# Optimization experiments

Measured on AMD Instinct MI355X. Metric: run time of the kernel, lower is better.

The kernel has to match this reference:

```python
import jax, jax.numpy as jnp
import numpy as np

B, S, H, NH = 4, 2048, 1024, 16
HD = H // NH


def setup_inputs() -> dict:
    key = jax.random.key(0)
    ks = jax.random.split(key, 8)
    x = jax.random.normal(ks[0], (B, S, H), dtype=jnp.float32)
    y = jax.random.normal(ks[1], (B, S, H), dtype=jnp.float32)
    mask = jnp.zeros((B, S), dtype=bool)  # key padding mask; True = masked
    s = 0.02
    Wq_w = jax.random.normal(ks[2], (H, H), dtype=jnp.float32) * s
    Wq_b = jnp.zeros((H,), dtype=jnp.float32)
    Wkv_w = jax.random.normal(ks[3], (H, 2 * H), dtype=jnp.float32) * s
    Wkv_b = jnp.zeros((2 * H,), dtype=jnp.float32)
    Wo_w = jax.random.normal(ks[4], (H, H), dtype=jnp.float32) * s
    Wo_b = jnp.zeros((H,), dtype=jnp.float32)
    return {"x": x, "y": y, "mask": mask, "Wq_w": Wq_w, "Wq_b": Wq_b,
            "Wkv_w": Wkv_w, "Wkv_b": Wkv_b, "Wo_w": Wo_w, "Wo_b": Wo_b}


def reference(x, y, mask, Wq_w, Wq_b, Wkv_w, Wkv_b, Wo_w, Wo_b):
    b, s, c = x.shape
    # q: [B, NH, S, HD]
    q = (x @ Wq_w + Wq_b).reshape(b, s, NH, HD).transpose(0, 2, 1, 3)
    # kv: [B, S, 2, NH, HD] -> k, v: [B, NH, S, HD]
    kv = (y @ Wkv_w + Wkv_b).reshape(b, s, 2, NH, HD)
    k = kv[:, :, 0].transpose(0, 2, 1, 3)
    v = kv[:, :, 1].transpose(0, 2, 1, 3)
    attn = jnp.einsum("bhqd,bhkd->bhqk", q, k) / jnp.sqrt(jnp.float32(HD))
    causal = jnp.triu(jnp.ones((s, s), dtype=bool), k=1)  # True above diag = masked
    combined = causal[None, None, :, :] | mask[:, None, None, :]
    attn = jnp.where(combined, -jnp.inf, attn)
    attn = jax.nn.softmax(attn, axis=-1)
    # dropout is identity in eval mode
    out = jnp.einsum("bhqk,bhkd->bhqd", attn, v)
    out = out.transpose(0, 2, 1, 3).reshape(b, s, c)
    return out @ Wo_w + Wo_b
```

## Files before the change

### kernel.cpp

```cpp
#include <hip/hip_runtime.h>


#define Bv   4
#define Sv   2048
#define Hv   1024
#define NHv  16
#define HDv  64

typedef __attribute__((ext_vector_type(8))) short s16x8;
typedef __attribute__((ext_vector_type(4))) short s16x4;
typedef __attribute__((ext_vector_type(4))) float f32x4;

__device__ __forceinline__ short f2bf(float f) {
  unsigned u = __float_as_uint(f);
  unsigned r = (u + 0x7fffu + ((u >> 16) & 1u)) >> 16;
  return (short)r;
}

#if __has_builtin(__builtin_amdgcn_exp2f)
#define EXP2(x) __builtin_amdgcn_exp2f(x)
#else
#define EXP2(x) exp2f(x)
#endif

__device__ __forceinline__ void gl_lds16(const short* g, short* l) {
  __builtin_amdgcn_global_load_lds(
      (const __attribute__((address_space(1))) unsigned int*)g,
      (__attribute__((address_space(3))) unsigned int*)l, 16, 0, 0);
}

__global__ __launch_bounds__(256) void cvt2_bf16(const float* __restrict__ x,
                                                 const float* __restrict__ y,
                                                 short* __restrict__ Xb,
                                                 short* __restrict__ Yb, int nper) {
  int half = gridDim.x >> 1;
  int bid = blockIdx.x;
  const float* in = (bid < half) ? x : y;
  short* out = (bid < half) ? Xb : Yb;
  int lb = (bid < half) ? bid : bid - half;
  int i = (lb * 256 + threadIdx.x) * 4;
  if (i < nper) {
    float4 v = *(const float4*)&in[i];
    short r0 = f2bf(v.x), r1 = f2bf(v.y), r2 = f2bf(v.z), r3 = f2bf(v.w);
    unsigned long long pk = (unsigned long long)(unsigned short)r0
                          | ((unsigned long long)(unsigned short)r1 << 16)
                          | ((unsigned long long)(unsigned short)r2 << 32)
                          | ((unsigned long long)(unsigned short)r3 << 48);
    *(unsigned long long*)&out[i] = pk;
  }
}

__global__ __launch_bounds__(256)
void tcvt3(const float* __restrict__ Wq, const float* __restrict__ Wkv,
           const float* __restrict__ Wo, short* __restrict__ Wt,
           short* __restrict__ Wot) {
  __shared__ float tile[32][33];
  int bx = blockIdx.x;
  const float* in;
  short* out;
  int C, cx;
  if (bx < 32)       { in = Wq;  out = Wt;                          C = 1024; cx = bx; }
  else if (bx < 96)  { in = Wkv; out = Wt + (size_t)Hv * Hv;        C = 2048; cx = bx - 32; }
  else               { in = Wo;  out = Wot;                         C = 1024; cx = bx - 96; }
  const int R = 1024;
  int tx = threadIdx.x & 31, ty = threadIdx.x >> 5;
  int c0 = cx * 32, r0 = blockIdx.y * 32;
#pragma unroll
  for (int i = 0; i < 32; i += 8)
    tile[ty + i][tx] = in[(size_t)(r0 + ty + i) * C + c0 + tx];
  __syncthreads();
#pragma unroll
  for (int i = 0; i < 32; i += 8)
    out[(size_t)(c0 + ty + i) * R + r0 + tx] = f2bf(tile[tx][ty + i]);
}

__global__ __launch_bounds__(256)
void gemm_qkv(const short* __restrict__ Xb, const short* __restrict__ Yb,
              const short* __restrict__ Wt, const float* __restrict__ Wqb,
              const float* __restrict__ Wkvb, short* __restrict__ Qb,
              short* __restrict__ Kb, short* __restrict__ Vt) {
  __shared__ union SMem {
    struct { short A[2][128 * 64]; short B[2][128 * 64]; } g;
    short ep[128 * 136];
  } sm;
  const int tid = threadIdx.x;
  const int w = tid >> 6, l = tid & 63;
  const int wr = w >> 1, wc = w & 1;
  const int m0 = blockIdx.x * 128, n0 = blockIdx.y * 128;
  const short* A = (n0 < 1024) ? Xb : Yb;
  const int sel = n0 >> 10;

  auto STAGE = [&](int k0, int bi) {
#pragma unroll
    for (int i = 0; i < 4; ++i) {
      int c = tid + i * 256;
      int r = c >> 3;
      int u = (c & 7) ^ (r & 7);
      gl_lds16(&A[(size_t)(m0 + r) * Hv + k0 + u * 8], &sm.g.A[bi][c * 8]);
      gl_lds16(&Wt[(size_t)(n0 + r) * Hv + k0 + u * 8], &sm.g.B[bi][c * 8]);
    }
  };

  f32x4 acc[4][4] = {};

  auto KSTEP = [&](int kt) {
    const int buf = kt & 1;
#pragma unroll
    for (int kk = 0; kk < 64; kk += 32) {
      s16x8 af[4], bf[4];
#pragma unroll
      for (int m = 0; m < 4; ++m) {
        int row = wr * 64 + m * 16 + (l & 15);
        int sb = (row * 128 + kk * 2 + ((l >> 4) << 4)) ^ ((row & 7) << 4);
        af[m] = *(s16x8*)((char*)sm.g.A[buf] + sb);
      }
#pragma unroll
      for (int n = 0; n < 4; ++n) {
        int row = wc * 64 + n * 16 + (l & 15);
        int sb = (row * 128 + kk * 2 + ((l >> 4) << 4)) ^ ((row & 7) << 4);
        bf[n] = *(s16x8*)((char*)sm.g.B[buf] + sb);
      }
#pragma unroll
      for (int m = 0; m < 4; ++m)
#pragma unroll
        for (int n = 0; n < 4; ++n)
          acc[m][n] = __builtin_amdgcn_mfma_f32_16x16x32_bf16(af[m], bf[n], acc[m][n], 0, 0, 0);
    }
  };

  STAGE(0, 0);
  STAGE(64, 1);

  for (int kt = 0; kt < 15; ++kt) {
    asm volatile("s_waitcnt vmcnt(8)" ::: "memory");
    __builtin_amdgcn_s_barrier();
    __builtin_amdgcn_sched_barrier(0);
    KSTEP(kt);
    __builtin_amdgcn_s_barrier();
    __builtin_amdgcn_sched_barrier(0);
    if (kt + 2 < 16) STAGE((kt + 2) * 64, kt & 1);
  }
  asm volatile("s_waitcnt vmcnt(0)" ::: "memory");
  __builtin_amdgcn_s_barrier();
  __builtin_amdgcn_sched_barrier(0);
  KSTEP(15);
  __syncthreads();

  const int b = m0 >> 11, s0 = m0 & (Sv - 1);
  if (sel < 2) {
    const float scale = (sel == 0) ? 0.1803368801f : 1.0f;
    const float* bias = (sel == 0) ? Wqb : (Wkvb + (n0 - 1024));
#pragma unroll
    for (int m = 0; m < 4; ++m)
#pragma unroll
      for (int n = 0; n < 4; ++n) {
        int scol = wc * 64 + n * 16 + (l & 15);
#pragma unroll
        for (int e = 0; e < 4; ++e) {
          int srow = wr * 64 + m * 16 + ((l >> 4) << 2) + e;
          float v = (acc[m][n][e] + bias[scol]) * scale;
          sm.ep[srow * 136 + scol] = f2bf(v);
        }
      }
    __syncthreads();
    short* dst = sel ? Kb : Qb;
    const int hbase = (n0 & 1023) >> 6;
#pragma unroll
    for (int p = 0; p < 8; ++p) {
      int u = p * 256 + tid;
      int row = u >> 4, hf = (u >> 3) & 1, sub = u & 7;
      s16x8 vdat = *(s16x8*)&sm.ep[row * 136 + hf * 64 + sub * 8];
      *(s16x8*)&dst[(((size_t)(b * NHv + hbase + hf)) * Sv + s0 + row) * HDv + sub * 8] = vdat;
    }
  } else {
    const float* bias = Wkvb + (n0 - 1024);
#pragma unroll
    for (int m = 0; m < 4; ++m)
#pragma unroll
      for (int n = 0; n < 4; ++n) {
        int scol = wc * 64 + n * 16 + (l & 15);
        int srow0 = wr * 64 + m * 16 + ((l >> 4) << 2);
        s16x4 t;
#pragma unroll
        for (int e = 0; e < 4; ++e) t[e] = f2bf(acc[m][n][e] + bias[scol]);
        *(s16x4*)&sm.ep[scol * 136 + srow0] = t;
      }
    __syncthreads();
    const int hbase = (n0 - 2048) >> 6;
#pragma unroll
    for (int p = 0; p < 8; ++p) {
      int u = p * 256 + tid;
      int col = u >> 4, seg = u & 15;
      s16x8 vdat = *(s16x8*)&sm.ep[col * 136 + seg * 8];
      *(s16x8*)&Vt[(((size_t)(b * NHv + hbase + (col >> 6))) * HDv + (col & 63)) * Sv + s0 + seg * 8] = vdat;
    }
  }
}

__global__ __launch_bounds__(256)
void gemm_out(const short* __restrict__ A, const short* __restrict__ Bt,
              const float* __restrict__ bias, float* __restrict__ outf) {
  __shared__ short Alds[2][128 * 64];
  __shared__ short Blds[2][128 * 64];
  const int tid = threadIdx.x;
  const int w = tid >> 6, l = tid & 63;
  const int wr = w >> 1, wc = w & 1;
  const int m0 = blockIdx.x * 128, n0 = blockIdx.y * 128;

  auto STAGE = [&](int k0, int bi) {
#pragma unroll
    for (int i = 0; i < 4; ++i) {
      int c = tid + i * 256;
      int r = c >> 3;
      int u = (c & 7) ^ (r & 7);
      gl_lds16(&A[(size_t)(m0 + r) * Hv + k0 + u * 8], &Alds[bi][c * 8]);
      gl_lds16(&Bt[(size_t)(n0 + r) * Hv + k0 + u * 8], &Blds[bi][c * 8]);
    }
  };

  f32x4 acc[4][4] = {};

  STAGE(0, 0);
  __syncthreads();
  for (int kt = 0; kt < 16; ++kt) {
    const int buf = kt & 1;
    if (kt < 15) STAGE((kt + 1) * 64, buf ^ 1);
#pragma unroll
    for (int kk = 0; kk < 64; kk += 32) {
      s16x8 af[4], bf[4];
#pragma unroll
      for (int m = 0; m < 4; ++m) {
        int row = wr * 64 + m * 16 + (l & 15);
        int sb = (row * 128 + kk * 2 + ((l >> 4) << 4)) ^ ((row & 7) << 4);
        af[m] = *(s16x8*)((char*)Alds[buf] + sb);
      }
#pragma unroll
      for (int n = 0; n < 4; ++n) {
        int row = wc * 64 + n * 16 + (l & 15);
        int sb = (row * 128 + kk * 2 + ((l >> 4) << 4)) ^ ((row & 7) << 4);
        bf[n] = *(s16x8*)((char*)Blds[buf] + sb);
      }
#pragma unroll
      for (int m = 0; m < 4; ++m)
#pragma unroll
        for (int n = 0; n < 4; ++n)
          acc[m][n] = __builtin_amdgcn_mfma_f32_16x16x32_bf16(af[m], bf[n], acc[m][n], 0, 0, 0);
    }
    __syncthreads();
  }

#pragma unroll
  for (int m = 0; m < 4; ++m)
#pragma unroll
    for (int n = 0; n < 4; ++n)
#pragma unroll
      for (int e = 0; e < 4; ++e) {
        int gr = m0 + wr * 64 + m * 16 + ((l >> 4) << 2) + e;
        int gc = n0 + wc * 64 + n * 16 + (l & 15);
        outf[(size_t)gr * Hv + gc] = acc[m][n][e] + bias[gc];
      }
}

__global__ __launch_bounds__(512)
void attn_mfma(const short* __restrict__ Q, const short* __restrict__ Kb,
               const short* __restrict__ Vt, const unsigned char* __restrict__ msk,
               short* __restrict__ AO) {
  __shared__ short Klds[2][64 * 64];
  __shared__ short Vlds[2][64 * 64];
  __shared__ short Plds[8 * 32 * 64];
  __shared__ unsigned long long mword[2];

  const int tid = threadIdx.x;
  const int w = tid >> 6, l = tid & 63;
  const int il = l & 15, g = l >> 4;
  const int bh = blockIdx.x & 63;
  const int qb = 7 - (blockIdx.x >> 6);
  const int b = bh >> 4, h = bh & 15;
  const int q0 = qb * 256 + w * 32;

  int kvA0[4], pfA0[2];
#pragma unroll
  for (int n = 0; n < 4; ++n) {
    int row = n * 16 + il;
    kvA0[n] = row * 128 + ((g << 4) ^ ((row & 7) << 4));
  }
#pragma unroll
  for (int m = 0; m < 2; ++m) {
    int row = m * 16 + il;
    pfA0[m] = row * 128 + ((g << 4) ^ ((row & 7) << 4));
  }
  const int swzq = (il & 7) << 4;
  const int g8 = g << 3;

  s16x8 qf[2][2];
  const short* qbase = &Q[((size_t)bh * Sv + q0) * HDv];
#pragma unroll
  for (int m = 0; m < 2; ++m)
#pragma unroll
    for (int kk = 0; kk < 2; ++kk)
      qf[m][kk] = *(const s16x8*)&qbase[(m * 16 + il) * 64 + kk * 32 + g8];

  s16x8 onesf;
#pragma unroll
  for (int e2 = 0; e2 < 8; ++e2) onesf[e2] = (short)0x3F80;

  f32x4 oacc[2][4] = {};
  f32x4 lacc[2] = {};
  const f32x4 cinit = {-16.f, -16.f, -16.f, -16.f};

  char* const pbase = (char*)Plds + w * 4096;
  const short* kg0 = &Kb[(size_t)bh * Sv * HDv];
  const short* vg0 = &Vt[(size_t)bh * HDv * Sv];
  const int nkt = qb * 4 + 4;

  auto stageKV = [&](int t, int bufi) {
    const short* kg = kg0 + (size_t)t * 64 * HDv;
    const short* vg = vg0 + t * 64;
    int c = tid;
    int r = c >> 3;
    int u = (c & 7) ^ (r & 7);
    gl_lds16(&kg[(size_t)r * HDv + u * 8], &Klds[bufi][c * 8]);
    gl_lds16(&vg[(size_t)r * Sv + u * 8], &Vlds[bufi][c * 8]);
  };

  stageKV(0, 0);
  if (w == 0) {
    unsigned long long mwb = __ballot(msk[b * Sv + l] != 0);
    if (l == 0) mword[0] = mwb;
  }
  __syncthreads();

  for (int kt = 0; kt < nkt; ++kt) {
    const int k0 = kt * 64;
    const int buf = kt & 1;
    if (kt + 1 < nkt) {
      stageKV(kt + 1, buf ^ 1);
      if (w == 0) {
        unsigned long long mwb = __ballot(msk[b * Sv + (kt + 1) * 64 + l] != 0);
        if (l == 0) mword[buf ^ 1] = mwb;
      }
    }

    if (k0 <= q0 + 31) {
      const unsigned long long mw = mword[buf];
      const char* kldsb = (const char*)Klds[buf];
      const char* vldsb = (const char*)Vlds[buf];
      f32x4 sacc[4][2];
#pragma unroll
      for (int n = 0; n < 4; ++n)
#pragma unroll
        for (int m = 0; m < 2; ++m)
          sacc[n][m] = cinit;
      __builtin_amdgcn_s_setprio(1);
#pragma unroll
      for (int kk = 0; kk < 2; ++kk) {
        s16x8 kf[4];
#pragma unroll
        for (int n = 0; n < 4; ++n)
          kf[n] = *(s16x8*)(kldsb + (kvA0[n] ^ (kk << 6)));
#pragma unroll
        for (int n = 0; n < 4; ++n)
#pragma unroll
          for (int m = 0; m < 2; ++m)
            sacc[n][m] = __builtin_amdgcn_mfma_f32_16x16x32_bf16(kf[n], qf[m][kk], sacc[n][m], 0, 0, 0);
      }
      __builtin_amdgcn_s_setprio(0);

      if ((k0 + 63 > q0) || (mw != 0)) {
#pragma unroll
        for (int n = 0; n < 4; ++n)
#pragma unroll
          for (int m = 0; m < 2; ++m)
#pragma unroll
            for (int e = 0; e < 4; ++e) {
              int klocal = n * 16 + (g << 2) + e;
              int qg = q0 + m * 16 + il;
              bool bad = (k0 + klocal > qg) || ((mw >> klocal) & 1ull);
              if (bad) sacc[n][m][e] = -1e30f;
            }
      }

#pragma unroll
      for (int kk = 0; kk < 2; ++kk) {
#pragma unroll
        for (int m = 0; m < 2; ++m) {
          int pwb = (m * 16 + il) * 128;
#pragma unroll
          for (int n = kk * 2; n < kk * 2 + 2; ++n) {
            s16x4 t;
#pragma unroll
            for (int e = 0; e < 4; ++e) {
              float pv = EXP2(sacc[n][m][e]);
              t[e] = (short)(__float_as_uint(pv) >> 16);
            }
            *(s16x4*)(pbase + pwb + (((n << 5) + g8) ^ swzq)) = t;
          }
        }
        s16x8 pf[2], vf[4];
#pragma unroll
        for (int m = 0; m < 2; ++m)
          pf[m] = *(s16x8*)(pbase + (pfA0[m] ^ (kk << 6)));
#pragma unroll
        for (int n = 0; n < 4; ++n)
          vf[n] = *(s16x8*)(vldsb + (kvA0[n] ^ (kk << 6)));
        __builtin_amdgcn_s_setprio(1);
#pragma unroll
        for (int m = 0; m < 2; ++m) {
#pragma unroll
          for (int n = 0; n < 4; ++n)
            oacc[m][n] = __builtin_amdgcn_mfma_f32_16x16x32_bf16(pf[m], vf[n], oacc[m][n], 0, 0, 0);
          lacc[m] = __builtin_amdgcn_mfma_f32_16x16x32_bf16(pf[m], onesf, lacc[m], 0, 0, 0);
        }
        __builtin_amdgcn_s_setprio(0);
      }
    }
    __syncthreads();
  }

#pragma unroll
  for (int m = 0; m < 2; ++m)
#pragma unroll
    for (int e = 0; e < 4; ++e) {
      float inv = 1.f / lacc[m][e];
#pragma unroll
      for (int n = 0; n < 4; ++n) {
        int qg = q0 + m * 16 + (g << 2) + e;
        int dcol = n * 16 + il;
        AO[((size_t)b * Sv + qg) * Hv + h * HDv + dcol] = f2bf(oacc[m][n][e] * inv);
      }
    }
}

extern "C" void kernel_launch(void* const* d_in, const int* in_sizes, int n_in,
                              void* d_out, int out_size, void* d_ws, size_t ws_size,
                              hipStream_t stream) {
  (void)in_sizes; (void)n_in; (void)out_size; (void)ws_size;
  const float* x    = (const float*)d_in[0];
  const float* y    = (const float*)d_in[1];
  const unsigned char* msk = (const unsigned char*)d_in[2];
  const float* Wq   = (const float*)d_in[3];
  const float* Wqb  = (const float*)d_in[4];
  const float* Wkv  = (const float*)d_in[5];
  const float* Wkvb = (const float*)d_in[6];
  const float* Wo   = (const float*)d_in[7];
  const float* Wob  = (const float*)d_in[8];
  float* out = (float*)d_out;

  char* p = (char*)d_ws;
  auto alloc = [&](size_t bytes) {
    char* r = p;
    p += (bytes + 255) & ~(size_t)255;
    return r;
  };
  const size_t MT = (size_t)Bv * Sv;
  short* Xb   = (short*)alloc(MT * Hv * 2);
  short* Yb   = (short*)alloc(MT * Hv * 2);
  short* Wt   = (short*)alloc((size_t)3 * Hv * Hv * 2);
  short* Wot  = (short*)alloc((size_t)Hv * Hv * 2);
  short* Qb   = (short*)alloc(MT * Hv * 2);
  short* Kb   = (short*)alloc(MT * Hv * 2);
  short* Vb   = (short*)alloc(MT * Hv * 2);
  short* AO   = (short*)alloc(MT * Hv * 2);

  const int n_x = (int)(MT * Hv);
  cvt2_bf16<<<2 * (n_x / 1024), 256, 0, stream>>>(x, y, Xb, Yb, n_x);
  tcvt3<<<dim3(128, 32), 256, 0, stream>>>(Wq, Wkv, Wo, Wt, Wot);

  gemm_qkv<<<dim3(64, 24), 256, 0, stream>>>(Xb, Yb, Wt, Wqb, Wkvb, Qb, Kb, Vb);

  attn_mfma<<<8 * 64, 512, 0, stream>>>(Qb, Kb, Vb, msk, AO);

  gemm_out<<<dim3(64, 8), 256, 0, stream>>>(AO, Wot, Wob, out);
}
```

Before: 158.2 us.

## Deepen GEMM and attention global-to-LDS pipelines with prefetch distance two

Both the projection GEMM and the attention kernel now issue two tiles ahead and wait with partial vmcnt counts plus raw s_barrier, instead of prefetching one tile and using full __syncthreads. The intent is to keep a load in flight across each compute step so global-to-LDS latency is hidden. The attention kernel also drops the shared mask-word LDS staging and has each wave ballot its mask byte directly. The hand-counted vmcnt values must match the number of outstanding loads per thread. The mask load in the compute step adds a global read on the critical path.

```diff
diff --git a/kernel.cpp b/kernel.cpp
--- a/kernel.cpp
+++ b/kernel.cpp
@@ -220,11 +220,8 @@
 
   f32x4 acc[4][4] = {};
 
-  STAGE(0, 0);
-  __syncthreads();
-  for (int kt = 0; kt < 16; ++kt) {
+  auto KSTEP = [&](int kt) {
     const int buf = kt & 1;
-    if (kt < 15) STAGE((kt + 1) * 64, buf ^ 1);
 #pragma unroll
     for (int kk = 0; kk < 64; kk += 32) {
       s16x8 af[4], bf[4];
@@ -246,8 +243,24 @@
         for (int n = 0; n < 4; ++n)
           acc[m][n] = __builtin_amdgcn_mfma_f32_16x16x32_bf16(af[m], bf[n], acc[m][n], 0, 0, 0);
     }
-    __syncthreads();
-  }
+  };
+
+  STAGE(0, 0);
+  STAGE(64, 1);
+
+  for (int kt = 0; kt < 15; ++kt) {
+    asm volatile("s_waitcnt vmcnt(8)" ::: "memory");
+    __builtin_amdgcn_s_barrier();
+    __builtin_amdgcn_sched_barrier(0);
+    KSTEP(kt);
+    __builtin_amdgcn_s_barrier();
+    __builtin_amdgcn_sched_barrier(0);
+    if (kt + 2 < 16) STAGE((kt + 2) * 64, kt & 1);
+  }
+  asm volatile("s_waitcnt vmcnt(0)" ::: "memory");
+  __builtin_amdgcn_s_barrier();
+  __builtin_amdgcn_sched_barrier(0);
+  KSTEP(15);
 
 #pragma unroll
   for (int m = 0; m < 4; ++m)
@@ -268,7 +281,6 @@
   __shared__ short Klds[2][64 * 64];
   __shared__ short Vlds[2][64 * 64];
   __shared__ short Plds[8 * 32 * 64];
-  __shared__ unsigned long long mword[2];
 
   const int tid = threadIdx.x;
   const int w = tid >> 6, l = tid & 63;
@@ -311,6 +323,7 @@
   char* const pbase = (char*)Plds + w * 4096;
   const short* kg0 = &Kb[(size_t)bh * Sv * HDv];
   const short* vg0 = &Vt[(size_t)bh * HDv * Sv];
+  const unsigned char* mrow = &msk[b * Sv + l];
   const int nkt = qb * 4 + 4;
 
   auto stageKV = [&](int t, int bufi) {
@@ -323,99 +336,101 @@
     gl_lds16(&vg[(size_t)r * Sv + u * 8], &Vlds[bufi][c * 8]);
   };
 
-  stageKV(0, 0);
-  if (w == 0) {
-    unsigned long long mwb = __ballot(msk[b * Sv + l] != 0);
-    if (l == 0) mword[0] = mwb;
-  }
-  __syncthreads();
-
-  for (int kt = 0; kt < nkt; ++kt) {
+  auto COMPUTE = [&](int kt) {
     const int k0 = kt * 64;
     const int buf = kt & 1;
-    if (kt + 1 < nkt) {
-      stageKV(kt + 1, buf ^ 1);
-      if (w == 0) {
-        unsigned long long mwb = __ballot(msk[b * Sv + (kt + 1) * 64 + l] != 0);
-        if (l == 0) mword[buf ^ 1] = mwb;
-      }
-    }
-
-    if (k0 <= q0 + 31) {
-      const unsigned long long mw = mword[buf];
-      const char* kldsb = (const char*)Klds[buf];
-      const char* vldsb = (const char*)Vlds[buf];
-      f32x4 sacc[4][2];
+    if (k0 > q0 + 31) return;
+    const unsigned char mb = mrow[k0];
+    const char* kldsb = (const char*)Klds[buf];
+    const char* vldsb = (const char*)Vlds[buf];
+    f32x4 sacc[4][2];
+#pragma unroll
+    for (int n = 0; n < 4; ++n)
+#pragma unroll
+      for (int m = 0; m < 2; ++m)
+        sacc[n][m] = cinit;
+    __builtin_amdgcn_s_setprio(1);
+#pragma unroll
+    for (int kk = 0; kk < 2; ++kk) {
+      s16x8 kf[4];
 #pragma unroll
       for (int n = 0; n < 4; ++n)
+        kf[n] = *(s16x8*)(kldsb + (kvA0[n] ^ (kk << 6)));
+#pragma unroll
+      for (int n = 0; n < 4; ++n)
 #pragma unroll
         for (int m = 0; m < 2; ++m)
-          sacc[n][m] = cinit;
+          sacc[n][m] = __builtin_amdgcn_mfma_f32_16x16x32_bf16(kf[n], qf[m][kk], sacc[n][m], 0, 0, 0);
+    }
+    __builtin_amdgcn_s_setprio(0);
+
+    const unsigned long long mw = __ballot(mb != 0);
+
+    if ((k0 + 63 > q0) || (mw != 0)) {
+#pragma unroll
+      for (int n = 0; n < 4; ++n)
+#pragma unroll
+        for (int m = 0; m < 2; ++m)
+#pragma unroll
+          for (int e = 0; e < 4; ++e) {
+            int klocal = n * 16 + (g << 2) + e;
+            int qg = q0 + m * 16 + il;
+            bool bad = (k0 + klocal > qg) || ((mw >> klocal) & 1ull);
+            if (bad) sacc[n][m][e] = -1e30f;
+          }
+    }
+
+#pragma unroll
+    for (int kk = 0; kk < 2; ++kk) {
+#pragma unroll
+      for (int m = 0; m < 2; ++m) {
+        int pwb = (m * 16 + il) * 128;
+#pragma unroll
+        for (int n = kk * 2; n < kk * 2 + 2; ++n) {
+          s16x4 t;
+#pragma unroll
+          for (int e = 0; e < 4; ++e) {
+            float pv = EXP2(sacc[n][m][e]);
+            t[e] = (short)(__float_as_uint(pv) >> 16);
+          }
+          *(s16x4*)(pbase + pwb + (((n << 5) + g8) ^ swzq)) = t;
+        }
+      }
+      s16x8 pf[2], vf[4];
+#pragma unroll
+      for (int m = 0; m < 2; ++m)
+        pf[m] = *(s16x8*)(pbase + (pfA0[m] ^ (kk << 6)));
+#pragma unroll
+      for (int n = 0; n < 4; ++n)
+        vf[n] = *(s16x8*)(vldsb + (kvA0[n] ^ (kk << 6)));
       __builtin_amdgcn_s_setprio(1);
 #pragma unroll
-      for (int kk = 0; kk < 2; ++kk) {
-        s16x8 kf[4];
+      for (int m = 0; m < 2; ++m) {
 #pragma unroll
         for (int n = 0; n < 4; ++n)
-          kf[n] = *(s16x8*)(kldsb + (kvA0[n] ^ (kk << 6)));
-#pragma unroll
-        for (int n = 0; n < 4; ++n)
-#pragma unroll
-          for (int m = 0; m < 2; ++m)
-            sacc[n][m] = __builtin_amdgcn_mfma_f32_16x16x32_bf16(kf[n], qf[m][kk], sacc[n][m], 0, 0, 0);
+          oacc[m][n] = __builtin_amdgcn_mfma_f32_16x16x32_bf16(pf[m], vf[n], oacc[m][n], 0, 0, 0);
+        lacc[m] = __builtin_amdgcn_mfma_f32_16x16x32_bf16(pf[m], onesf, lacc[m], 0, 0, 0);
       }
       __builtin_amdgcn_s_setprio(0);
-
-      if ((k0 + 63 > q0) || (mw != 0)) {
-#pragma unroll
-        for (int n = 0; n < 4; ++n)
-#pragma unroll
-          for (int m = 0; m < 2; ++m)
-#pragma unroll
-            for (int e = 0; e < 4; ++e) {
-              int klocal = n * 16 + (g << 2) + e;
-              int qg = q0 + m * 16 + il;
-              bool bad = (k0 + klocal > qg) || ((mw >> klocal) & 1ull);
-              if (bad) sacc[n][m][e] = -1e30f;
-            }
-      }
-
-#pragma unroll
-      for (int kk = 0; kk < 2; ++kk) {
-#pragma unroll
-        for (int m = 0; m < 2; ++m) {
-          int pwb = (m * 16 + il) * 128;
-#pragma unroll
-          for (int n = kk * 2; n < kk * 2 + 2; ++n) {
-            s16x4 t;
-#pragma unroll
-            for (int e = 0; e < 4; ++e) {
-              float pv = EXP2(sacc[n][m][e]);
-              t[e] = (short)(__float_as_uint(pv) >> 16);
-            }
-            *(s16x4*)(pbase + pwb + (((n << 5) + g8) ^ swzq)) = t;
-          }
-        }
-        s16x8 pf[2], vf[4];
-#pragma unroll
-        for (int m = 0; m < 2; ++m)
-          pf[m] = *(s16x8*)(pbase + (pfA0[m] ^ (kk << 6)));
-#pragma unroll
-        for (int n = 0; n < 4; ++n)
-          vf[n] = *(s16x8*)(vldsb + (kvA0[n] ^ (kk << 6)));
-        __builtin_amdgcn_s_setprio(1);
-#pragma unroll
-        for (int m = 0; m < 2; ++m) {
-#pragma unroll
-          for (int n = 0; n < 4; ++n)
-            oacc[m][n] = __builtin_amdgcn_mfma_f32_16x16x32_bf16(pf[m], vf[n], oacc[m][n], 0, 0, 0);
-          lacc[m] = __builtin_amdgcn_mfma_f32_16x16x32_bf16(pf[m], onesf, lacc[m], 0, 0, 0);
-        }
-        __builtin_amdgcn_s_setprio(0);
-      }
-    }
-    __syncthreads();
-  }
+    }
+  };
+
+  stageKV(0, 0);
+  stageKV(1, 1);
+
+  for (int kt = 0; kt < nkt - 1; ++kt) {
+    asm volatile("s_waitcnt vmcnt(2)" ::: "memory");
+    __builtin_amdgcn_s_barrier();
+    __builtin_amdgcn_sched_barrier(0);
+    COMPUTE(kt);
+    __builtin_amdgcn_s_barrier();
+    __builtin_amdgcn_sched_barrier(0);
+    if (kt + 2 < nkt) stageKV(kt + 2, kt & 1);
+  }
+  asm volatile("s_waitcnt vmcnt(0)" ::: "memory");
+  __builtin_amdgcn_s_barrier();
+  __builtin_amdgcn_sched_barrier(0);
+  COMPUTE(nkt - 1);
 
 #pragma unroll
   for (int m = 0; m < 2; ++m)
```

New measurement: 160.7 us. Within noise of the previous version (+1.6%).
